# Kernel tuning notes

Measured on AMD Instinct MI355X. Metric: run time of the kernel, lower is better.

## Reference

```python
import jax, jax.numpy as jnp
import numpy as np

DIM = 64   # voxel grid resolution per axis
C = 64     # channels (C_in == num_outputs, required by residual add)
N = 200000 # number of points
EPS = 1e-3 # keras BatchNormalization default epsilon

def _bn(x, g, b, m, v):
    # inference-mode batch norm
    return (x - m) * jax.lax.rsqrt(v + EPS) * g + b

def _conv3d_relu(x, k, b):
    # x: [1,X,Y,Z,Cin], k: [3,3,3,Cin,Cout] (DHWIO), 'same' padding, relu activation
    y = jax.lax.conv_general_dilated(x, k, (1, 1, 1), 'SAME',
        dimension_numbers=('NDHWC', 'DHWIO', 'NDHWC'))
    return jax.nn.relu(y + b)

def _trilinear(grid, pts):
    # grid: [X,Y,Z,C], pts: [N,3] in voxel coordinates
    dmax = jnp.asarray(grid.shape[:3], pts.dtype) - 1.0
    p = jnp.clip(pts, 0.0, dmax)
    f = jnp.floor(p)
    t = p - f  # [N,3] fractional part
    i0 = f.astype(jnp.int32)
    i1 = jnp.minimum(i0 + 1, jnp.asarray(grid.shape[:3], jnp.int32) - 1)
    out = jnp.zeros((pts.shape[0], grid.shape[-1]), grid.dtype)
    for dx in (0, 1):
        for dy in (0, 1):
            for dz in (0, 1):
                ix = i1[:, 0] if dx else i0[:, 0]
                iy = i1[:, 1] if dy else i0[:, 1]
                iz = i1[:, 2] if dz else i0[:, 2]
                w = ((t[:, 0] if dx else 1.0 - t[:, 0])
                     * (t[:, 1] if dy else 1.0 - t[:, 1])
                     * (t[:, 2] if dz else 1.0 - t[:, 2]))
                out = out + w[:, None] * grid[ix, iy, iz]
    return out

def setup_inputs():
    key = jax.random.key(0)
    ks = jax.random.split(key, 10)
    inputs = jax.random.normal(ks[0], (N, C), jnp.float32)
    # pt_coords already scaled into voxel space (VOXEL_SIZE_INV folded in)
    pt_coords = jax.random.uniform(ks[1], (N, 3), jnp.float32) * (DIM - 1)
    voxel_indexes = jax.random.randint(ks[2], (N, 3), 0, DIM)
    pts_per_voxel_inv = jax.random.uniform(ks[3], (1, DIM, DIM, DIM, 1), jnp.float32)
    s = 1.0 / np.sqrt(C)
    w_mlp = jax.random.normal(ks[4], (C, C), jnp.float32) * s
    b_mlp = jnp.zeros((C,), jnp.float32)
    sk = 1.0 / np.sqrt(27 * C)
    k1 = jax.random.normal(ks[5], (3, 3, 3, C, C), jnp.float32) * sk
    cb1 = jnp.zeros((C,), jnp.float32)
    k2 = jax.random.normal(ks[6], (3, 3, 3, C, C), jnp.float32) * sk
    cb2 = jnp.zeros((C,), jnp.float32)
    def bn_params(k):
        a, b_, c = jax.random.split(k, 3)
        g = 1.0 + 0.1 * jax.random.normal(a, (C,), jnp.float32)
        be = 0.1 * jax.random.normal(b_, (C,), jnp.float32)
        m = 0.1 * jax.random.normal(c, (C,), jnp.float32)
        v = jnp.ones((C,), jnp.float32)
        return g, be, m, v
    g0, be0, m0, v0 = bn_params(ks[7])
    g1, be1, m1, v1 = bn_params(ks[8])
    g2, be2, m2, v2 = bn_params(ks[9])
    return dict(inputs=inputs, pt_coords=pt_coords, voxel_indexes=voxel_indexes,
                pts_per_voxel_inv=pts_per_voxel_inv, w_mlp=w_mlp, b_mlp=b_mlp,
                g0=g0, be0=be0, m0=m0, v0=v0, k1=k1, cb1=cb1, g1=g1, be1=be1,
                m1=m1, v1=v1, k2=k2, cb2=cb2, g2=g2, be2=be2, m2=m2, v2=v2)

def reference(inputs, pt_coords, voxel_indexes, pts_per_voxel_inv, w_mlp, b_mlp,
              g0, be0, m0, v0, k1, cb1, g1, be1, m1, v1, k2, cb2, g2, be2, m2, v2):
    # point branch: Dense(relu) + BN
    mlp_out = _bn(jax.nn.relu(inputs @ w_mlp + b_mlp), g0, be0, m0, v0)
    # voxelize: scatter_nd adds duplicate-index contributions
    voxels = jnp.zeros((DIM, DIM, DIM, C), inputs.dtype).at[
        voxel_indexes[:, 0], voxel_indexes[:, 1], voxel_indexes[:, 2]].add(inputs)
    voxels = voxels[None] * pts_per_voxel_inv  # per-voxel mean normalization
    # voxel branch: two Conv3D(relu)+BN
    h = _bn(_conv3d_relu(voxels, k1, cb1), g1, be1, m1, v1)
    h = _bn(_conv3d_relu(h, k2, cb2), g2, be2, m2, v2)
    # devoxelize: trilinear gather back to points (coords already in voxel space)
    vox_out = _trilinear(h[0], pt_coords)
    return mlp_out + vox_out
```

## Files before the change

### kernel.cpp

```cpp
#include <hip/hip_runtime.h>
#include <hip/hip_bf16.h>

#define DIMV 64
#define CH 64
#define EPSB 1e-3f

using bf16x8 = __attribute__((ext_vector_type(8))) short;
using f32x16 = __attribute__((ext_vector_type(16))) float;

__device__ __forceinline__ unsigned short f2bf(float f) {
    union { float f; unsigned u; } x; x.f = f;
    unsigned r = x.u + 0x7fff + ((x.u >> 16) & 1);
    return (unsigned short)(r >> 16);
}
__device__ __forceinline__ float bf2f(unsigned short u) {
    union { unsigned u; float f; } x; x.u = ((unsigned)u) << 16;
    return x.f;
}

__global__ void scatter_kernel(const float* __restrict__ x, const int* __restrict__ idx,
                               float* __restrict__ grid, int n_total) {
    int tid = blockIdx.x * blockDim.x + threadIdx.x;
    if (tid >= n_total) return;
    int n = tid >> 6, c = tid & 63;
    int ix = idx[n * 3 + 0], iy = idx[n * 3 + 1], iz = idx[n * 3 + 2];
    atomicAdd(&grid[(size_t)(((ix * DIMV) + iy) * DIMV + iz) * CH + c], x[tid]);
}

__global__ void wprep_kernel(const float* __restrict__ K, unsigned short* __restrict__ wbuf) {
    int t = blockIdx.x * 256 + threadIdx.x;
    if (t >= 27 * 4 * 2 * 64 * 8) return;
    int j = t & 7;
    int l = (t >> 3) & 63;
    int nt = (t >> 9) & 1;
    int kkl = (t >> 10) & 3;
    int d = t >> 12;
    int ci = kkl * 16 + (l >> 5) * 8 + j;
    int co = nt * 32 + (l & 31);
    wbuf[t] = f2bf(K[((size_t)d * 64 + ci) * 64 + co]);
}

__global__ void wprep_mlp(const float* __restrict__ W, unsigned short* __restrict__ wm) {
    int t = blockIdx.x * 256 + threadIdx.x;
    if (t >= 4 * 2 * 64 * 8) return;
    int j = t & 7;
    int l = (t >> 3) & 63;
    int nt = (t >> 9) & 1;
    int kkl = (t >> 10) & 3;
    int ci = kkl * 16 + (l >> 5) * 8 + j;
    int co = nt * 32 + (l & 31);
    wm[t] = f2bf(W[(size_t)ci * 64 + co]);
}

template <int FUSE>
__global__ __launch_bounds__(256) void conv_mfma(
    const unsigned short* __restrict__ Gb, const float* __restrict__ Gf,
    const float* __restrict__ inv, const unsigned short* __restrict__ wbuf,
    const float* __restrict__ cb, const float* __restrict__ g,
    const float* __restrict__ be, const float* __restrict__ m,
    const float* __restrict__ v, unsigned short* __restrict__ out) {
    __shared__ __align__(16) unsigned short slab[612 * 128];
    const int tid = threadIdx.x;
    const int lane = tid & 63;
    const int w = tid >> 6;
    const int lz = lane & 31;
    const int kg = lane >> 5;
    const int BX = blockIdx.x, BY = blockIdx.y, BZ = blockIdx.z;
    const int x0 = 4 * BX - 1, y0 = 4 * BY - 1;
    const int zbase = 32 * BZ - 1;

    for (int it = 0; it < 39; ++it) {
        int idx = it * 256 + tid;
        if (idx < 9792) {
            int s = idx & 15;
            int r = idx >> 4;
            int zp = r % 17;
            int ryx = r / 17;
            int xx = x0 + ryx / 6;
            int yy = y0 + ryx % 6;
            int cp = s ^ (zp & 15);
            int c = cp >> 1, p = cp & 1;
            int zz = zbase + 2 * zp + p;
            if (FUSE) {
                __align__(16) unsigned short tmp[8] = {0, 0, 0, 0, 0, 0, 0, 0};
                if ((unsigned)xx < DIMV && (unsigned)yy < DIMV && (unsigned)zz < DIMV) {
                    int vox = ((xx * DIMV) + yy) * DIMV + zz;
                    const float* src = Gf + (size_t)vox * CH + c * 8;
                    float sc = inv[vox];
#pragma unroll
                    for (int j = 0; j < 8; ++j) tmp[j] = f2bf(src[j] * sc);
                }
                *(int4*)(slab + (size_t)idx * 8) = *(const int4*)tmp;
            } else {
                int4 val = make_int4(0, 0, 0, 0);
                if ((unsigned)xx < DIMV && (unsigned)yy < DIMV && (unsigned)zz < DIMV)
                    val = *(const int4*)(Gb + (size_t)(((xx * DIMV) + yy) * DIMV + zz) * CH + c * 8);
                *(int4*)(slab + (size_t)idx * 8) = val;
            }
        }
    }
    __syncthreads();

    f32x16 acc[4][2];
#pragma unroll
    for (int yc = 0; yc < 4; ++yc)
#pragma unroll
        for (int nt = 0; nt < 2; ++nt)
#pragma unroll
            for (int r = 0; r < 16; ++r) acc[yc][nt][r] = 0.f;

#pragma unroll
    for (int dx = 0; dx < 3; ++dx)
#pragma unroll
        for (int dz = 0; dz < 3; ++dz) {
            const int zval = lz + dz;
            const int zp = zval >> 1, p = zval & 1;
            const int rb = ((w + dx) * 6) * 17 + zp;
#pragma unroll
            for (int kkl = 0; kkl < 4; ++kkl) {
                const int slot = ((kkl * 2 + kg) * 2 + p) ^ (zp & 15);
                bf16x8 a[6];
#pragma unroll
                for (int ys = 0; ys < 6; ++ys)
                    a[ys] = *(const bf16x8*)(slab + (rb + ys * 17) * 128 + slot * 8);
                bf16x8 bb[3][2];
#pragma unroll
                for (int dy = 0; dy < 3; ++dy) {
                    const unsigned short* wd =
                        wbuf + (size_t)(dx * 9 + dy * 3 + dz) * 4096 + (kkl * 2) * 512 + lane * 8;
                    bb[dy][0] = *(const bf16x8*)(wd);
                    bb[dy][1] = *(const bf16x8*)(wd + 512);
                }
#pragma unroll
                for (int dy = 0; dy < 3; ++dy)
#pragma unroll
                    for (int yc = 0; yc < 4; ++yc) {
                        acc[yc][0] = __builtin_amdgcn_mfma_f32_32x32x16_bf16(
                            a[yc + dy], bb[dy][0], acc[yc][0], 0, 0, 0);
                        acc[yc][1] = __builtin_amdgcn_mfma_f32_32x32x16_bf16(
                            a[yc + dy], bb[dy][1], acc[yc][1], 0, 0, 0);
                    }
            }
        }

    const int x_out = 4 * BX + w;
#pragma unroll
    for (int yc = 0; yc < 4; ++yc) {
        int y_out = 4 * BY + yc;
#pragma unroll
        for (int nt = 0; nt < 2; ++nt) {
            int co = nt * 32 + lz;
            float scale = g[co] * rsqrtf(v[co] + EPSB);
            float shift = be[co] - m[co] * scale;
            float bias = cb[co];
            size_t base = (size_t)((x_out * DIMV) + y_out) * DIMV * CH + co;
#pragma unroll
            for (int r = 0; r < 16; ++r) {
                int zrow = (r & 3) + 8 * (r >> 2) + 4 * kg;
                int z = BZ * 32 + zrow;
                float val = fmaxf(acc[yc][nt][r] + bias, 0.f) * scale + shift;
                out[base + (size_t)z * CH] = f2bf(val);
            }
        }
    }
}

__global__ __launch_bounds__(256) void mlp_gather(
    const float* __restrict__ x, const unsigned short* __restrict__ wfrag,
    const float* __restrict__ b, const float* __restrict__ g,
    const float* __restrict__ be, const float* __restrict__ m,
    const float* __restrict__ v, const unsigned short* __restrict__ grid,
    const float* __restrict__ pts, float* __restrict__ out, int npts) {
    __shared__ float lds[128 * 64];
    const int w = threadIdx.x >> 6;
    const int lane = threadIdx.x & 63;
    const int col = lane & 31;
    const int kg = lane >> 5;
    const int p0 = (blockIdx.x * 4 + w) * 32;

    if (p0 < npts) {
        bf16x8 a[4];
        const float* xr = x + (size_t)(p0 + col) * CH + kg * 8;
#pragma unroll
        for (int kk = 0; kk < 4; ++kk) {
            const float* p = xr + kk * 16;
            bf16x8 t;
#pragma unroll
            for (int j = 0; j < 8; ++j) t[j] = (short)f2bf(p[j]);
            a[kk] = t;
        }
        f32x16 acc[2];
#pragma unroll
        for (int nt = 0; nt < 2; ++nt)
#pragma unroll
            for (int r = 0; r < 16; ++r) acc[nt][r] = 0.f;
#pragma unroll
        for (int kk = 0; kk < 4; ++kk) {
            bf16x8 b0 = *(const bf16x8*)(wfrag + (kk * 2 + 0) * 512 + lane * 8);
            bf16x8 b1 = *(const bf16x8*)(wfrag + (kk * 2 + 1) * 512 + lane * 8);
            acc[0] = __builtin_amdgcn_mfma_f32_32x32x16_bf16(a[kk], b0, acc[0], 0, 0, 0);
            acc[1] = __builtin_amdgcn_mfma_f32_32x32x16_bf16(a[kk], b1, acc[1], 0, 0, 0);
        }
#pragma unroll
        for (int nt = 0; nt < 2; ++nt) {
            int co = nt * 32 + col;
            float scale = g[co] * rsqrtf(v[co] + EPSB);
            float shift = be[co] - m[co] * scale;
            float bias = b[co];
#pragma unroll
            for (int r = 0; r < 16; ++r) {
                int row = (r & 3) + 8 * (r >> 2) + 4 * kg;
                float val = fmaxf(acc[nt][r] + bias, 0.f) * scale + shift;
                lds[(w * 32 + row) * 64 + co] = val;
            }
        }
    }
    __syncthreads();

    const int pblk = blockIdx.x * 128;
#pragma unroll 4
    for (int i = 0; i < 32; ++i) {
        int idx = i * 256 + threadIdx.x;
        int pl = idx >> 6;
        int c = idx & 63;
        int pt = pblk + pl;
        if (pt >= npts) break;
        float px = fminf(fmaxf(pts[pt * 3 + 0], 0.f), (float)(DIMV - 1));
        float py = fminf(fmaxf(pts[pt * 3 + 1], 0.f), (float)(DIMV - 1));
        float pz = fminf(fmaxf(pts[pt * 3 + 2], 0.f), (float)(DIMV - 1));
        float fx = floorf(px), fy = floorf(py), fz = floorf(pz);
        float tx = px - fx, ty = py - fy, tz = pz - fz;
        int x0 = (int)fx, y0 = (int)fy, z0 = (int)fz;
        int x1 = min(x0 + 1, DIMV - 1), y1 = min(y0 + 1, DIMV - 1), z1 = min(z0 + 1, DIMV - 1);
        float wx0 = 1.f - tx, wy0 = 1.f - ty, wz0 = 1.f - tz;
        float acc = lds[pl * 64 + c];
        acc = fmaf(wx0 * wy0 * wz0, bf2f(grid[(size_t)(((x0 * DIMV) + y0) * DIMV + z0) * CH + c]), acc);
        acc = fmaf(wx0 * wy0 * tz,  bf2f(grid[(size_t)(((x0 * DIMV) + y0) * DIMV + z1) * CH + c]), acc);
        acc = fmaf(wx0 * ty * wz0,  bf2f(grid[(size_t)(((x0 * DIMV) + y1) * DIMV + z0) * CH + c]), acc);
        acc = fmaf(wx0 * ty * tz,   bf2f(grid[(size_t)(((x0 * DIMV) + y1) * DIMV + z1) * CH + c]), acc);
        acc = fmaf(tx * wy0 * wz0,  bf2f(grid[(size_t)(((x1 * DIMV) + y0) * DIMV + z0) * CH + c]), acc);
        acc = fmaf(tx * wy0 * tz,   bf2f(grid[(size_t)(((x1 * DIMV) + y0) * DIMV + z1) * CH + c]), acc);
        acc = fmaf(tx * ty * wz0,   bf2f(grid[(size_t)(((x1 * DIMV) + y1) * DIMV + z0) * CH + c]), acc);
        acc = fmaf(tx * ty * tz,    bf2f(grid[(size_t)(((x1 * DIMV) + y1) * DIMV + z1) * CH + c]), acc);
        out[(size_t)pt * CH + c] = acc;
    }
}

extern "C" void kernel_launch(void* const* d_in, const int* in_sizes, int n_in,
                              void* d_out, int out_size, void* d_ws, size_t ws_size,
                              hipStream_t stream) {
    const float* inputs = (const float*)d_in[0];
    const float* pt_coords = (const float*)d_in[1];
    const int* voxel_indexes = (const int*)d_in[2];
    const float* ppvi = (const float*)d_in[3];
    const float* w_mlp = (const float*)d_in[4];
    const float* b_mlp = (const float*)d_in[5];
    const float* g0 = (const float*)d_in[6];
    const float* be0 = (const float*)d_in[7];
    const float* m0 = (const float*)d_in[8];
    const float* v0 = (const float*)d_in[9];
    const float* k1 = (const float*)d_in[10];
    const float* cb1 = (const float*)d_in[11];
    const float* g1 = (const float*)d_in[12];
    const float* be1 = (const float*)d_in[13];
    const float* m1 = (const float*)d_in[14];
    const float* v1 = (const float*)d_in[15];
    const float* k2 = (const float*)d_in[16];
    const float* cb2 = (const float*)d_in[17];
    const float* g2 = (const float*)d_in[18];
    const float* be2 = (const float*)d_in[19];
    const float* m2 = (const float*)d_in[20];
    const float* v2 = (const float*)d_in[21];
    float* out = (float*)d_out;

    char* ws = (char*)d_ws;
    float* A = (float*)ws;
    unsigned short* G3 = (unsigned short*)ws;
    unsigned short* G2 = (unsigned short*)(ws + 67108864);
    unsigned short* wbuf1 = (unsigned short*)(ws + 100663296);
    unsigned short* wbuf2 = (unsigned short*)(ws + 100884480);
    unsigned short* wmlp = (unsigned short*)(ws + 101105664);

    const int n_total = in_sizes[0];
    const int npts = n_total / CH;
    const int nblk = (n_total + 255) / 256;
    const size_t grid_elems = (size_t)DIMV * DIMV * DIMV * CH;

    hipMemsetAsync(A, 0, grid_elems * sizeof(float), stream);
    wprep_mlp<<<16, 256, 0, stream>>>(w_mlp, wmlp);
    wprep_kernel<<<432, 256, 0, stream>>>(k1, wbuf1);
    wprep_kernel<<<432, 256, 0, stream>>>(k2, wbuf2);
    scatter_kernel<<<nblk, 256, 0, stream>>>(inputs, voxel_indexes, A, n_total);

    dim3 cgrid(16, 16, 2);
    conv_mfma<1><<<cgrid, 256, 0, stream>>>(nullptr, A, ppvi, wbuf1, cb1, g1, be1, m1, v1, G2);
    conv_mfma<0><<<cgrid, 256, 0, stream>>>(G2, nullptr, nullptr, wbuf2, cb2, g2, be2, m2, v2, G3);

    mlp_gather<<<(npts + 127) / 128, 256, 0, stream>>>(
        inputs, wmlp, b_mlp, g0, be0, m0, v0, G3, pt_coords, out, npts);
}
```

Measured before the change: 301.9 us.

## Split conv MFMA work over 8 waves with double-buffered weight prefetch

Conv blocks now run 8 waves instead of 4. Each wave computes a 1x2 (x,y) patch of output columns rather than a 1x4 row, which halves the per-wave accumulators and raises occupancy. The 27 taps are flattened into a single loop whose start offset is staggered per wave, spreading weight reads across the L2. The next tap's weight fragments are prefetched into a second register buffer while the current tap computes. The cost is more A-fragment reloads from LDS per MFMA, since each loaded row now feeds fewer y outputs.

```diff
diff --git a/kernel.cpp b/kernel.cpp
--- a/kernel.cpp
+++ b/kernel.cpp
@@ -53,7 +53,7 @@
 }
 
 template <int FUSE>
-__global__ __launch_bounds__(256) void conv_mfma(
+__global__ __launch_bounds__(512) void conv_mfma(
     const unsigned short* __restrict__ Gb, const float* __restrict__ Gf,
     const float* __restrict__ inv, const unsigned short* __restrict__ wbuf,
     const float* __restrict__ cb, const float* __restrict__ g,
@@ -63,14 +63,16 @@
     const int tid = threadIdx.x;
     const int lane = tid & 63;
     const int w = tid >> 6;
+    const int cx = w >> 1;
+    const int cy0 = 2 * (w & 1);
     const int lz = lane & 31;
     const int kg = lane >> 5;
     const int BX = blockIdx.x, BY = blockIdx.y, BZ = blockIdx.z;
     const int x0 = 4 * BX - 1, y0 = 4 * BY - 1;
     const int zbase = 32 * BZ - 1;
 
-    for (int it = 0; it < 39; ++it) {
-        int idx = it * 256 + tid;
+    for (int it = 0; it < 20; ++it) {
+        int idx = it * 512 + tid;
         if (idx < 9792) {
             int s = idx & 15;
             int r = idx >> 4;
@@ -101,52 +103,61 @@
     }
     __syncthreads();
 
-    f32x16 acc[4][2];
-#pragma unroll
-    for (int yc = 0; yc < 4; ++yc)
+    f32x16 acc[2][2];
+#pragma unroll
+    for (int ct = 0; ct < 2; ++ct)
 #pragma unroll
         for (int nt = 0; nt < 2; ++nt)
 #pragma unroll
-            for (int r = 0; r < 16; ++r) acc[yc][nt][r] = 0.f;
-
-#pragma unroll
-    for (int dx = 0; dx < 3; ++dx)
-#pragma unroll
-        for (int dz = 0; dz < 3; ++dz) {
-            const int zval = lz + dz;
-            const int zp = zval >> 1, p = zval & 1;
-            const int rb = ((w + dx) * 6) * 17 + zp;
-#pragma unroll
-            for (int kkl = 0; kkl < 4; ++kkl) {
-                const int slot = ((kkl * 2 + kg) * 2 + p) ^ (zp & 15);
-                bf16x8 a[6];
-#pragma unroll
-                for (int ys = 0; ys < 6; ++ys)
-                    a[ys] = *(const bf16x8*)(slab + (rb + ys * 17) * 128 + slot * 8);
-                bf16x8 bb[3][2];
-#pragma unroll
-                for (int dy = 0; dy < 3; ++dy) {
-                    const unsigned short* wd =
-                        wbuf + (size_t)(dx * 9 + dy * 3 + dz) * 4096 + (kkl * 2) * 512 + lane * 8;
-                    bb[dy][0] = *(const bf16x8*)(wd);
-                    bb[dy][1] = *(const bf16x8*)(wd + 512);
-                }
-#pragma unroll
-                for (int dy = 0; dy < 3; ++dy)
-#pragma unroll
-                    for (int yc = 0; yc < 4; ++yc) {
-                        acc[yc][0] = __builtin_amdgcn_mfma_f32_32x32x16_bf16(
-                            a[yc + dy], bb[dy][0], acc[yc][0], 0, 0, 0);
-                        acc[yc][1] = __builtin_amdgcn_mfma_f32_32x32x16_bf16(
-                            a[yc + dy], bb[dy][1], acc[yc][1], 0, 0, 0);
-                    }
-            }
-        }
-
-    const int x_out = 4 * BX + w;
-#pragma unroll
-    for (int yc = 0; yc < 4; ++yc) {
-        int y_out = 4 * BY + yc;
+            for (int r = 0; r < 16; ++r) acc[ct][nt][r] = 0.f;
+
+    const int doff = w * 3;
+
+    bf16x8 bfr0[8], bfr1[8];
+    auto issueB = [&](bf16x8 (&B)[8], int d) {
+        const unsigned short* wn = wbuf + (size_t)d * 4096 + lane * 8;
+#pragma unroll
+        for (int q = 0; q < 8; ++q) B[q] = *(const bf16x8*)(wn + q * 512);
+    };
+    auto stepCompute = [&](bf16x8 (&B)[8], int d) {
+        const int dx = d / 9, dy = (d / 3) % 3, dz = d % 3;
+        const int zval = lz + dz;
+        const int zp = zval >> 1, p = zval & 1;
+        const int rbase = ((cx + dx) * 6 + (cy0 + dy)) * 17 + zp;
+#pragma unroll
+        for (int kkl = 0; kkl < 4; ++kkl) {
+            const int slot = ((kkl * 2 + kg) * 2 + p) ^ (zp & 15);
+            bf16x8 a0 = *(const bf16x8*)(slab + rbase * 128 + slot * 8);
+            bf16x8 a1 = *(const bf16x8*)(slab + (rbase + 17) * 128 + slot * 8);
+            acc[0][0] = __builtin_amdgcn_mfma_f32_32x32x16_bf16(a0, B[kkl * 2 + 0], acc[0][0], 0, 0, 0);
+            acc[1][0] = __builtin_amdgcn_mfma_f32_32x32x16_bf16(a1, B[kkl * 2 + 0], acc[1][0], 0, 0, 0);
+            acc[0][1] = __builtin_amdgcn_mfma_f32_32x32x16_bf16(a0, B[kkl * 2 + 1], acc[0][1], 0, 0, 0);
+            acc[1][1] = __builtin_amdgcn_mfma_f32_32x32x16_bf16(a1, B[kkl * 2 + 1], acc[1][1], 0, 0, 0);
+        }
+    };
+
+    {
+        int d0 = __builtin_amdgcn_readfirstlane(doff);
+        issueB(bfr0, d0);
+    }
+#pragma unroll
+    for (int s = 0; s < 27; ++s) {
+        if (s < 26) {
+            int dn = doff + s + 1;
+            if (dn >= 27) dn -= 27;
+            dn = __builtin_amdgcn_readfirstlane(dn);
+            if (s & 1) issueB(bfr0, dn); else issueB(bfr1, dn);
+        }
+        int dc = doff + s;
+        if (dc >= 27) dc -= 27;
+        dc = __builtin_amdgcn_readfirstlane(dc);
+        if (s & 1) stepCompute(bfr1, dc); else stepCompute(bfr0, dc);
+    }
+
+    const int x_out = 4 * BX + cx;
+#pragma unroll
+    for (int ct = 0; ct < 2; ++ct) {
+        int y_out = 4 * BY + cy0 + ct;
 #pragma unroll
         for (int nt = 0; nt < 2; ++nt) {
             int co = nt * 32 + lz;
@@ -158,7 +169,7 @@
             for (int r = 0; r < 16; ++r) {
                 int zrow = (r & 3) + 8 * (r >> 2) + 4 * kg;
                 int z = BZ * 32 + zrow;
-                float val = fmaxf(acc[yc][nt][r] + bias, 0.f) * scale + shift;
+                float val = fmaxf(acc[ct][nt][r] + bias, 0.f) * scale + shift;
                 out[base + (size_t)z * CH] = f2bf(val);
             }
         }
@@ -293,8 +304,8 @@
     scatter_kernel<<<nblk, 256, 0, stream>>>(inputs, voxel_indexes, A, n_total);
 
     dim3 cgrid(16, 16, 2);
-    conv_mfma<1><<<cgrid, 256, 0, stream>>>(nullptr, A, ppvi, wbuf1, cb1, g1, be1, m1, v1, G2);
-    conv_mfma<0><<<cgrid, 256, 0, stream>>>(G2, nullptr, nullptr, wbuf2, cb2, g2, be2, m2, v2, G3);
+    conv_mfma<1><<<cgrid, 512, 0, stream>>>(nullptr, A, ppvi, wbuf1, cb1, g1, be1, m1, v1, G2);
+    conv_mfma<0><<<cgrid, 512, 0, stream>>>(G2, nullptr, nullptr, wbuf2, cb2, g2, be2, m2, v2, G3);
 
     mlp_gather<<<(npts + 127) / 128, 256, 0, stream>>>(
         inputs, wmlp, b_mlp, g0, be0, m0, v0, G3, pt_coords, out, npts);
```

Result: faster. 286.5 us (-5.1%).
